# Performance work log

Measured on AMD Instinct MI355X. Metric: run time of the kernel, lower is better.

The kernel has to match this reference:

```python
import jax, jax.numpy as jnp
import numpy as np

BLOCK_SIZES = [256] * 8            # sum = N_CTX = 2048
B, H, D = 2, 16, 64
N_CTX = sum(BLOCK_SIZES)
SPARSITY_PATTERN = 'block_causal'  # row_starts = 0, row_ends = end of own block


def _build_masks(block_sizes, pattern):
    cs = np.cumsum([0] + list(block_sizes))
    row_ends = np.concatenate([np.full(bs, cs[i + 1], dtype=np.int32)
                               for i, bs in enumerate(block_sizes)])
    if pattern == 'block_diagonal':
        row_starts = np.concatenate([np.full(bs, cs[i], dtype=np.int32)
                                     for i, bs in enumerate(block_sizes)])
    elif pattern == 'block_causal':
        row_starts = np.zeros_like(row_ends)
    else:
        raise ValueError(pattern)
    return jnp.asarray(row_starts), jnp.asarray(row_ends)


def setup_inputs() -> dict:
    key = jax.random.key(0)
    kq, kk, kv = jax.random.split(key, 3)
    q = jax.random.normal(kq, (B, H, N_CTX, D), dtype=jnp.float32)
    k = jax.random.normal(kk, (B, H, N_CTX, D), dtype=jnp.float32)
    v = jax.random.normal(kv, (B, H, N_CTX, D), dtype=jnp.float32)
    row_starts, row_ends = _build_masks(BLOCK_SIZES, SPARSITY_PATTERN)
    sm_scale = jnp.float32(1.0 / np.sqrt(D))
    return {"q": q, "k": k, "v": v, "sm_scale": sm_scale,
            "row_starts": row_starts, "row_ends": row_ends}


def reference(q, k, v, sm_scale, row_starts, row_ends):
    # q,k,v: [B,H,N,D]; per query row i, attend to kv cols in [row_starts[i], row_ends[i])
    n = q.shape[2]
    cols = jnp.arange(n, dtype=jnp.int32)
    allowed = (cols[None, :] >= row_starts[:, None]) & (cols[None, :] < row_ends[:, None])  # [N,N]
    scores = jnp.einsum('bhqd,bhkd->bhqk', q, k) * sm_scale
    neg = jnp.finfo(scores.dtype).min
    scores = jnp.where(allowed[None, None], scores, neg)
    p = jax.nn.softmax(scores, axis=-1)
    return jnp.einsum('bhqk,bhkd->bhqd', p, v)
```

## Files before the change

kernel.cpp:

```cpp
#include <hip/hip_runtime.h>


typedef short bf16x8 __attribute__((ext_vector_type(8)));
typedef float f32x4  __attribute__((ext_vector_type(4)));
typedef unsigned short u16;
typedef u16 u16x8 __attribute__((ext_vector_type(8)));

#define MFMA(A,B,C) __builtin_amdgcn_mfma_f32_16x16x32_bf16((A),(B),(C),0,0,0)

__device__ __forceinline__ u16 f2bf_rne(float f) {
    union { float f; unsigned u; } c; c.f = f;
    unsigned r = c.u + 0x7FFFu + ((c.u >> 16) & 1u);
    return (u16)(r >> 16);
}
__device__ __forceinline__ u16 f2bf_fast(float f) {
    union { float f; unsigned u; } c; c.f = f;
    return (u16)((c.u + 0x8000u) >> 16);
}

__global__ __launch_bounds__(256, 2)
void bsattn_fused(const float* __restrict__ Q, const float* __restrict__ K,
                  const float* __restrict__ V, const float* __restrict__ SC,
                  const int* __restrict__ RS, const int* __restrict__ RE,
                  float* __restrict__ O)
{
    constexpr int N = 2048, D = 64;
    int wg = blockIdx.x;
    int bh = wg & 31;
    int i0 = wg >> 5;
    int qsub = (i0 < 8) ? i0 : 23 - i0;
    int q0 = qsub << 7;

    int tid = threadIdx.x, wid = tid >> 6, lane = tid & 63;
    int n = lane & 15, g = lane >> 4;

    __shared__ __align__(16) u16 lsm[16384];
    __shared__ int sbi[8];

    int row0 = q0 + wid * 32 + n;
    int row1 = row0 + 16;
    int rs_l0 = RS[row0], re_l0 = RE[row0];
    int rs_l1 = RS[row1], re_l1 = RE[row1];
    int w_rs_min = min(rs_l0, rs_l1), w_rs_max = max(rs_l0, rs_l1);
    int w_re_min = min(re_l0, re_l1), w_re_max = max(re_l0, re_l1);
    #pragma unroll
    for (int o = 1; o < 16; o <<= 1) {
        w_rs_min = min(w_rs_min, __shfl_xor(w_rs_min, o));
        w_rs_max = max(w_rs_max, __shfl_xor(w_rs_max, o));
        w_re_min = min(w_re_min, __shfl_xor(w_re_min, o));
        w_re_max = max(w_re_max, __shfl_xor(w_re_max, o));
    }
    if (lane == 0) { sbi[wid * 2] = w_rs_min; sbi[wid * 2 + 1] = w_re_max; }

    float sscale = SC[0] * 1.44269504088896340736f;

    bf16x8 qA0, qA1, qB0, qB1;
    {
        const float* qp = Q + ((size_t)bh * N + row0) * D + g * 8;
        float4 a0 = *(const float4*)qp,        a1 = *(const float4*)(qp + 4);
        float4 b0 = *(const float4*)(qp + 32), b1 = *(const float4*)(qp + 36);
        qA0[0]=f2bf_rne(a0.x*sscale); qA0[1]=f2bf_rne(a0.y*sscale);
        qA0[2]=f2bf_rne(a0.z*sscale); qA0[3]=f2bf_rne(a0.w*sscale);
        qA0[4]=f2bf_rne(a1.x*sscale); qA0[5]=f2bf_rne(a1.y*sscale);
        qA0[6]=f2bf_rne(a1.z*sscale); qA0[7]=f2bf_rne(a1.w*sscale);
        qA1[0]=f2bf_rne(b0.x*sscale); qA1[1]=f2bf_rne(b0.y*sscale);
        qA1[2]=f2bf_rne(b0.z*sscale); qA1[3]=f2bf_rne(b0.w*sscale);
        qA1[4]=f2bf_rne(b1.x*sscale); qA1[5]=f2bf_rne(b1.y*sscale);
        qA1[6]=f2bf_rne(b1.z*sscale); qA1[7]=f2bf_rne(b1.w*sscale);
    }
    {
        const float* qp = Q + ((size_t)bh * N + row1) * D + g * 8;
        float4 a0 = *(const float4*)qp,        a1 = *(const float4*)(qp + 4);
        float4 b0 = *(const float4*)(qp + 32), b1 = *(const float4*)(qp + 36);
        qB0[0]=f2bf_rne(a0.x*sscale); qB0[1]=f2bf_rne(a0.y*sscale);
        qB0[2]=f2bf_rne(a0.z*sscale); qB0[3]=f2bf_rne(a0.w*sscale);
        qB0[4]=f2bf_rne(a1.x*sscale); qB0[5]=f2bf_rne(a1.y*sscale);
        qB0[6]=f2bf_rne(a1.z*sscale); qB0[7]=f2bf_rne(a1.w*sscale);
        qB1[0]=f2bf_rne(b0.x*sscale); qB1[1]=f2bf_rne(b0.y*sscale);
        qB1[2]=f2bf_rne(b0.z*sscale); qB1[3]=f2bf_rne(b0.w*sscale);
        qB1[4]=f2bf_rne(b1.x*sscale); qB1[5]=f2bf_rne(b1.y*sscale);
        qB1[6]=f2bf_rne(b1.z*sscale); qB1[7]=f2bf_rne(b1.w*sscale);
    }

    __syncthreads();
    int kst  = min(min(sbi[0], sbi[2]), min(sbi[4], sbi[6])) & ~63;
    int kend = max(max(sbi[1], sbi[3]), max(sbi[5], sbi[7]));
    int t0 = kst >> 6;
    int w  = (kend - kst + 63) >> 6;

    int rA   = ((n >> 2) << 3) + (n & 3);
    int phk  = (n & 3) + 4 * ((n >> 2) & 1);
    int osA0 = rA * 64 + ((g + phk) & 7) * 8;
    int osA1 = rA * 64 + ((g + 4 + phk) & 7) * 8;
    int ov0  = 4096 + n * 64 + ((    g + (n & 7)) & 7) * 8;
    int ov1  = 4096 + n * 64 + ((4 + g + (n & 7)) & 7) * 8;

    int key_l = tid >> 2, c2 = (tid & 3) << 1;
    int rotb  = (key_l & 3) + 4 * ((key_l >> 3) & 1);
    int kiA   = key_l * 64 + (((c2    ) + rotb) & 7) * 8;
    int kiB   = key_l * 64 + (((c2 + 1) + rotb) & 7) * 8;
    int kc    = lane >> 3, kw = lane & 7;
    const float* Kb = K + (size_t)bh * N * D;
    const float* Vb = V + (size_t)bh * N * D;

    f32x4 accA[4], accB[4];
    f32x4 acclA = {0.f,0.f,0.f,0.f}, acclB = {0.f,0.f,0.f,0.f};
    #pragma unroll
    for (int c = 0; c < 4; ++c) {
        accA[c] = (f32x4){0.f,0.f,0.f,0.f};
        accB[c] = (f32x4){0.f,0.f,0.f,0.f};
    }
    bf16x8 ones;
    #pragma unroll
    for (int j = 0; j < 8; ++j) ones[j] = (short)0x3F80;

    float4 kf0, kf1, kf2, kf3, vf0, vf1, vf2, vf3;

    auto stage_load = [&](int i) {
        if (i < w) {
            const float* kp = Kb + (size_t)(t0 + i) * 4096 + key_l * 64 + c2 * 8;
            kf0 = *(const float4*)kp;       kf1 = *(const float4*)(kp + 4);
            kf2 = *(const float4*)(kp + 8); kf3 = *(const float4*)(kp + 12);
            const float* vp = Vb + (size_t)(t0 + i) * 4096 + lane * 64 + wid * 16;
            vf0 = *(const float4*)vp;       vf1 = *(const float4*)(vp + 4);
            vf2 = *(const float4*)(vp + 8); vf3 = *(const float4*)(vp + 12);
        }
    };
    auto stage_write = [&](int i) {
        if (i < w) {
            u16* dst = &lsm[(i & 1) << 13];
            u16x8 a, b;
            a[0]=f2bf_rne(kf0.x); a[1]=f2bf_rne(kf0.y); a[2]=f2bf_rne(kf0.z); a[3]=f2bf_rne(kf0.w);
            a[4]=f2bf_rne(kf1.x); a[5]=f2bf_rne(kf1.y); a[6]=f2bf_rne(kf1.z); a[7]=f2bf_rne(kf1.w);
            b[0]=f2bf_rne(kf2.x); b[1]=f2bf_rne(kf2.y); b[2]=f2bf_rne(kf2.z); b[3]=f2bf_rne(kf2.w);
            b[4]=f2bf_rne(kf3.x); b[5]=f2bf_rne(kf3.y); b[6]=f2bf_rne(kf3.z); b[7]=f2bf_rne(kf3.w);
            *(u16x8*)&dst[kiA] = a;
            *(u16x8*)&dst[kiB] = b;
            float vy[16] = { vf0.x,vf0.y,vf0.z,vf0.w, vf1.x,vf1.y,vf1.z,vf1.w,
                             vf2.x,vf2.y,vf2.z,vf2.w, vf3.x,vf3.y,vf3.z,vf3.w };
            #pragma unroll
            for (int j = 0; j < 16; ++j) {
                int d = wid * 16 + j;
                dst[4096 + d * 64 + ((kc + (j & 7)) & 7) * 8 + kw] = f2bf_rne(vy[j]);
            }
        }
    };

    auto proc = [&](int kb, const u16* ls) {
        bool bdry = (kb < w_rs_max) || (kb + 64 > w_re_min);
        #pragma unroll
        for (int h = 0; h < 2; ++h) {
            int hb = h * 2048;
            bf16x8 k00 = *(const bf16x8*)&ls[hb + osA0];
            bf16x8 k01 = *(const bf16x8*)&ls[hb + osA1];
            bf16x8 k10 = *(const bf16x8*)&ls[hb + osA0 + 256];
            bf16x8 k11 = *(const bf16x8*)&ls[hb + osA1 + 256];
            f32x4 tA0 = {0.f,0.f,0.f,0.f}, tA1 = tA0, tB0 = tA0, tB1 = tA0;
            __builtin_amdgcn_s_setprio(1);
            tA0 = MFMA(k00, qA0, tA0); tA0 = MFMA(k01, qA1, tA0);
            tA1 = MFMA(k10, qA0, tA1); tA1 = MFMA(k11, qA1, tA1);
            tB0 = MFMA(k00, qB0, tB0); tB0 = MFMA(k01, qB1, tB0);
            tB1 = MFMA(k10, qB0, tB1); tB1 = MFMA(k11, qB1, tB1);
            __builtin_amdgcn_s_setprio(0);
            float sA[8], sB[8];
            #pragma unroll
            for (int r = 0; r < 4; ++r) {
                sA[r] = tA0[r]; sA[4 + r] = tA1[r];
                sB[r] = tB0[r]; sB[4 + r] = tB1[r];
            }
            if (bdry) {
                #pragma unroll
                for (int j = 0; j < 8; ++j) {
                    int key = kb + h * 32 + g * 8 + j;
                    if (key < rs_l0 || key >= re_l0) sA[j] = -1e30f;
                    if (key < rs_l1 || key >= re_l1) sB[j] = -1e30f;
                }
            }
            bf16x8 pA, pB;
            #pragma unroll
            for (int j = 0; j < 8; ++j) { float p = __builtin_amdgcn_exp2f(sA[j]); pA[j] = (short)f2bf_fast(p); }
            #pragma unroll
            for (int j = 0; j < 8; ++j) { float p = __builtin_amdgcn_exp2f(sB[j]); pB[j] = (short)f2bf_fast(p); }
            int ov = h ? ov1 : ov0;
            bf16x8 v0 = *(const bf16x8*)&ls[ov       ];
            bf16x8 v1 = *(const bf16x8*)&ls[ov + 1024];
            bf16x8 v2 = *(const bf16x8*)&ls[ov + 2048];
            bf16x8 v3 = *(const bf16x8*)&ls[ov + 3072];
            __builtin_amdgcn_s_setprio(1);
            accA[0] = MFMA(pA, v0, accA[0]);
            accA[1] = MFMA(pA, v1, accA[1]);
            accA[2] = MFMA(pA, v2, accA[2]);
            accA[3] = MFMA(pA, v3, accA[3]);
            acclA   = MFMA(pA, ones, acclA);
            accB[0] = MFMA(pB, v0, accB[0]);
            accB[1] = MFMA(pB, v1, accB[1]);
            accB[2] = MFMA(pB, v2, accB[2]);
            accB[3] = MFMA(pB, v3, accB[3]);
            acclB   = MFMA(pB, ones, acclB);
            __builtin_amdgcn_s_setprio(0);
        }
    };

    stage_load(0);
    stage_write(0);
    stage_load(1);
    for (int i = 0; i < w; ++i) {
        __syncthreads();
        proc(kst + (i << 6), &lsm[(i & 1) << 13]);
        stage_write(i + 1);
        stage_load(i + 2);
    }

    int rb = g << 2;
    {
        int orow = q0 + wid * 32 + rb;
        float* ob = O + ((size_t)bh * N + orow) * D + n;
        #pragma unroll
        for (int r = 0; r < 4; ++r) {
            float li = 1.0f / acclA[r];
            float* rp = ob + (size_t)r * D;
            rp[0]  = accA[0][r] * li;
            rp[16] = accA[1][r] * li;
            rp[32] = accA[2][r] * li;
            rp[48] = accA[3][r] * li;
        }
    }
    {
        int orow = q0 + wid * 32 + 16 + rb;
        float* ob = O + ((size_t)bh * N + orow) * D + n;
        #pragma unroll
        for (int r = 0; r < 4; ++r) {
            float li = 1.0f / acclB[r];
            float* rp = ob + (size_t)r * D;
            rp[0]  = accB[0][r] * li;
            rp[16] = accB[1][r] * li;
            rp[32] = accB[2][r] * li;
            rp[48] = accB[3][r] * li;
        }
    }
}

extern "C" void kernel_launch(void* const* d_in, const int* in_sizes, int n_in,
                              void* d_out, int out_size, void* d_ws, size_t ws_size,
                              hipStream_t stream) {
    const float* q  = (const float*)d_in[0];
    const float* k  = (const float*)d_in[1];
    const float* v  = (const float*)d_in[2];
    const float* sc = (const float*)d_in[3];
    const int* rs   = (const int*)d_in[4];
    const int* re   = (const int*)d_in[5];
    float* out      = (float*)d_out;

    bsattn_fused<<<dim3(512), dim3(256), 0, stream>>>(q, k, v, sc, rs, re, out);
}
```

Before: 130.8 us.

## Halve query tile to 64 rows, double grid, raise occupancy, reorder tile schedule

Each workgroup now handles 64 query rows (16 per wave) instead of 128, so the grid grows from 512 to 1024 workgroups and launch bounds ask for 4 blocks per CU. The tile order is remapped to put the longest causal query tiles first, which is meant to balance load. The prefetch depth in the K/V pipeline drops from two stages ahead to one, and each wave now holds a single Q fragment and one set of accumulators, which lowers register pressure. The cost is that every K/V tile is loaded and converted by twice as many workgroups, roughly doubling global traffic and conversion work per output row, and the shorter prefetch distance gives less time to hide load latency.

```diff
diff --git a/kernel.cpp b/kernel.cpp
--- a/kernel.cpp
+++ b/kernel.cpp
@@ -18,7 +18,7 @@
     return (u16)((c.u + 0x8000u) >> 16);
 }
 
-__global__ __launch_bounds__(256, 2)
+__global__ __launch_bounds__(256, 4)
 void bsattn_fused(const float* __restrict__ Q, const float* __restrict__ K,
                   const float* __restrict__ V, const float* __restrict__ SC,
                   const int* __restrict__ RS, const int* __restrict__ RE,
@@ -27,9 +27,11 @@
     constexpr int N = 2048, D = 64;
     int wg = blockIdx.x;
     int bh = wg & 31;
-    int i0 = wg >> 5;
-    int qsub = (i0 < 8) ? i0 : 23 - i0;
-    int q0 = qsub << 7;
+    int i0 = wg >> 5, kk = i0 & 7, rr = i0 >> 3;
+    int qt = (rr == 0) ? ((kk < 4) ? 28 + kk : 20 + kk)
+           : (rr == 1) ? ((kk < 4) ? 20 + kk : 12 + kk)
+           : (rr == 2) ? (8 + kk) : kk;
+    int q0 = qt << 6;
 
     int tid = threadIdx.x, wid = tid >> 6, lane = tid & 63;
     int n = lane & 15, g = lane >> 4;
@@ -37,12 +39,9 @@
     __shared__ __align__(16) u16 lsm[16384];
     __shared__ int sbi[8];
 
-    int row0 = q0 + wid * 32 + n;
-    int row1 = row0 + 16;
-    int rs_l0 = RS[row0], re_l0 = RE[row0];
-    int rs_l1 = RS[row1], re_l1 = RE[row1];
-    int w_rs_min = min(rs_l0, rs_l1), w_rs_max = max(rs_l0, rs_l1);
-    int w_re_min = min(re_l0, re_l1), w_re_max = max(re_l0, re_l1);
+    int myrow = q0 + wid * 16 + n;
+    int rs_l = RS[myrow], re_l = RE[myrow];
+    int w_rs_min = rs_l, w_rs_max = rs_l, w_re_min = re_l, w_re_max = re_l;
     #pragma unroll
     for (int o = 1; o < 16; o <<= 1) {
         w_rs_min = min(w_rs_min, __shfl_xor(w_rs_min, o));
@@ -54,32 +53,19 @@
 
     float sscale = SC[0] * 1.44269504088896340736f;
 
-    bf16x8 qA0, qA1, qB0, qB1;
+    bf16x8 qf0, qf1;
     {
-        const float* qp = Q + ((size_t)bh * N + row0) * D + g * 8;
+        const float* qp = Q + ((size_t)bh * N + myrow) * D + g * 8;
         float4 a0 = *(const float4*)qp,        a1 = *(const float4*)(qp + 4);
         float4 b0 = *(const float4*)(qp + 32), b1 = *(const float4*)(qp + 36);
-        qA0[0]=f2bf_rne(a0.x*sscale); qA0[1]=f2bf_rne(a0.y*sscale);
-        qA0[2]=f2bf_rne(a0.z*sscale); qA0[3]=f2bf_rne(a0.w*sscale);
-        qA0[4]=f2bf_rne(a1.x*sscale); qA0[5]=f2bf_rne(a1.y*sscale);
-        qA0[6]=f2bf_rne(a1.z*sscale); qA0[7]=f2bf_rne(a1.w*sscale);
-        qA1[0]=f2bf_rne(b0.x*sscale); qA1[1]=f2bf_rne(b0.y*sscale);
-        qA1[2]=f2bf_rne(b0.z*sscale); qA1[3]=f2bf_rne(b0.w*sscale);
-        qA1[4]=f2bf_rne(b1.x*sscale); qA1[5]=f2bf_rne(b1.y*sscale);
-        qA1[6]=f2bf_rne(b1.z*sscale); qA1[7]=f2bf_rne(b1.w*sscale);
-    }
-    {
-        const float* qp = Q + ((size_t)bh * N + row1) * D + g * 8;
-        float4 a0 = *(const float4*)qp,        a1 = *(const float4*)(qp + 4);
-        float4 b0 = *(const float4*)(qp + 32), b1 = *(const float4*)(qp + 36);
-        qB0[0]=f2bf_rne(a0.x*sscale); qB0[1]=f2bf_rne(a0.y*sscale);
-        qB0[2]=f2bf_rne(a0.z*sscale); qB0[3]=f2bf_rne(a0.w*sscale);
-        qB0[4]=f2bf_rne(a1.x*sscale); qB0[5]=f2bf_rne(a1.y*sscale);
-        qB0[6]=f2bf_rne(a1.z*sscale); qB0[7]=f2bf_rne(a1.w*sscale);
-        qB1[0]=f2bf_rne(b0.x*sscale); qB1[1]=f2bf_rne(b0.y*sscale);
-        qB1[2]=f2bf_rne(b0.z*sscale); qB1[3]=f2bf_rne(b0.w*sscale);
-        qB1[4]=f2bf_rne(b1.x*sscale); qB1[5]=f2bf_rne(b1.y*sscale);
-        qB1[6]=f2bf_rne(b1.z*sscale); qB1[7]=f2bf_rne(b1.w*sscale);
+        qf0[0]=f2bf_rne(a0.x*sscale); qf0[1]=f2bf_rne(a0.y*sscale);
+        qf0[2]=f2bf_rne(a0.z*sscale); qf0[3]=f2bf_rne(a0.w*sscale);
+        qf0[4]=f2bf_rne(a1.x*sscale); qf0[5]=f2bf_rne(a1.y*sscale);
+        qf0[6]=f2bf_rne(a1.z*sscale); qf0[7]=f2bf_rne(a1.w*sscale);
+        qf1[0]=f2bf_rne(b0.x*sscale); qf1[1]=f2bf_rne(b0.y*sscale);
+        qf1[2]=f2bf_rne(b0.z*sscale); qf1[3]=f2bf_rne(b0.w*sscale);
+        qf1[4]=f2bf_rne(b1.x*sscale); qf1[5]=f2bf_rne(b1.y*sscale);
+        qf1[6]=f2bf_rne(b1.z*sscale); qf1[7]=f2bf_rne(b1.w*sscale);
     }
 
     __syncthreads();
@@ -103,13 +89,9 @@
     const float* Kb = K + (size_t)bh * N * D;
     const float* Vb = V + (size_t)bh * N * D;
 
-    f32x4 accA[4], accB[4];
-    f32x4 acclA = {0.f,0.f,0.f,0.f}, acclB = {0.f,0.f,0.f,0.f};
-    #pragma unroll
-    for (int c = 0; c < 4; ++c) {
-        accA[c] = (f32x4){0.f,0.f,0.f,0.f};
-        accB[c] = (f32x4){0.f,0.f,0.f,0.f};
-    }
+    f32x4 acc[4], accl = {0.f, 0.f, 0.f, 0.f};
+    #pragma unroll
+    for (int c = 0; c < 4; ++c) acc[c] = (f32x4){0.f, 0.f, 0.f, 0.f};
     bf16x8 ones;
     #pragma unroll
     for (int j = 0; j < 8; ++j) ones[j] = (short)0x3F80;
@@ -147,96 +129,68 @@
     };
 
     auto proc = [&](int kb, const u16* ls) {
-        bool bdry = (kb < w_rs_max) || (kb + 64 > w_re_min);
+        float sc[16];
         #pragma unroll
         for (int h = 0; h < 2; ++h) {
             int hb = h * 2048;
-            bf16x8 k00 = *(const bf16x8*)&ls[hb + osA0];
-            bf16x8 k01 = *(const bf16x8*)&ls[hb + osA1];
-            bf16x8 k10 = *(const bf16x8*)&ls[hb + osA0 + 256];
-            bf16x8 k11 = *(const bf16x8*)&ls[hb + osA1 + 256];
-            f32x4 tA0 = {0.f,0.f,0.f,0.f}, tA1 = tA0, tB0 = tA0, tB1 = tA0;
+            f32x4 t0v = {0.f,0.f,0.f,0.f}, t1v = t0v;
             __builtin_amdgcn_s_setprio(1);
-            tA0 = MFMA(k00, qA0, tA0); tA0 = MFMA(k01, qA1, tA0);
-            tA1 = MFMA(k10, qA0, tA1); tA1 = MFMA(k11, qA1, tA1);
-            tB0 = MFMA(k00, qB0, tB0); tB0 = MFMA(k01, qB1, tB0);
-            tB1 = MFMA(k10, qB0, tB1); tB1 = MFMA(k11, qB1, tB1);
+            t0v = MFMA(*(const bf16x8*)&ls[hb + osA0],       qf0, t0v);
+            t0v = MFMA(*(const bf16x8*)&ls[hb + osA1],       qf1, t0v);
+            t1v = MFMA(*(const bf16x8*)&ls[hb + osA0 + 256], qf0, t1v);
+            t1v = MFMA(*(const bf16x8*)&ls[hb + osA1 + 256], qf1, t1v);
             __builtin_amdgcn_s_setprio(0);
-            float sA[8], sB[8];
             #pragma unroll
-            for (int r = 0; r < 4; ++r) {
-                sA[r] = tA0[r]; sA[4 + r] = tA1[r];
-                sB[r] = tB0[r]; sB[4 + r] = tB1[r];
-            }
-            if (bdry) {
+            for (int r = 0; r < 4; ++r) { sc[h*8 + r] = t0v[r]; sc[h*8 + 4 + r] = t1v[r]; }
+        }
+        if (kb < w_rs_max || kb + 64 > w_re_min) {
+            #pragma unroll
+            for (int h = 0; h < 2; ++h)
                 #pragma unroll
                 for (int j = 0; j < 8; ++j) {
                     int key = kb + h * 32 + g * 8 + j;
-                    if (key < rs_l0 || key >= re_l0) sA[j] = -1e30f;
-                    if (key < rs_l1 || key >= re_l1) sB[j] = -1e30f;
+                    if (key < rs_l || key >= re_l) sc[h*8 + j] = -1e30f;
                 }
-            }
-            bf16x8 pA, pB;
-            #pragma unroll
-            for (int j = 0; j < 8; ++j) { float p = __builtin_amdgcn_exp2f(sA[j]); pA[j] = (short)f2bf_fast(p); }
-            #pragma unroll
-            for (int j = 0; j < 8; ++j) { float p = __builtin_amdgcn_exp2f(sB[j]); pB[j] = (short)f2bf_fast(p); }
+        }
+        bf16x8 pf0, pf1;
+        #pragma unroll
+        for (int j = 0; j < 8; ++j) { float p = __builtin_amdgcn_exp2f(sc[j]);     pf0[j] = (short)f2bf_fast(p); }
+        #pragma unroll
+        for (int j = 0; j < 8; ++j) { float p = __builtin_amdgcn_exp2f(sc[8 + j]); pf1[j] = (short)f2bf_fast(p); }
+        #pragma unroll
+        for (int h = 0; h < 2; ++h) {
+            const bf16x8& pf = h ? pf1 : pf0;
             int ov = h ? ov1 : ov0;
-            bf16x8 v0 = *(const bf16x8*)&ls[ov       ];
-            bf16x8 v1 = *(const bf16x8*)&ls[ov + 1024];
-            bf16x8 v2 = *(const bf16x8*)&ls[ov + 2048];
-            bf16x8 v3 = *(const bf16x8*)&ls[ov + 3072];
             __builtin_amdgcn_s_setprio(1);
-            accA[0] = MFMA(pA, v0, accA[0]);
-            accA[1] = MFMA(pA, v1, accA[1]);
-            accA[2] = MFMA(pA, v2, accA[2]);
-            accA[3] = MFMA(pA, v3, accA[3]);
-            acclA   = MFMA(pA, ones, acclA);
-            accB[0] = MFMA(pB, v0, accB[0]);
-            accB[1] = MFMA(pB, v1, accB[1]);
-            accB[2] = MFMA(pB, v2, accB[2]);
-            accB[3] = MFMA(pB, v3, accB[3]);
-            acclB   = MFMA(pB, ones, acclB);
+            acc[0] = MFMA(pf, *(const bf16x8*)&ls[ov       ], acc[0]);
+            acc[1] = MFMA(pf, *(const bf16x8*)&ls[ov + 1024], acc[1]);
+            acc[2] = MFMA(pf, *(const bf16x8*)&ls[ov + 2048], acc[2]);
+            acc[3] = MFMA(pf, *(const bf16x8*)&ls[ov + 3072], acc[3]);
+            accl   = MFMA(pf, ones, accl);
             __builtin_amdgcn_s_setprio(0);
         }
     };
 
     stage_load(0);
     stage_write(0);
-    stage_load(1);
     for (int i = 0; i < w; ++i) {
         __syncthreads();
+        stage_load(i + 1);
         proc(kst + (i << 6), &lsm[(i & 1) << 13]);
         stage_write(i + 1);
-        stage_load(i + 2);
     }
 
     int rb = g << 2;
-    {
-        int orow = q0 + wid * 32 + rb;
-        float* ob = O + ((size_t)bh * N + orow) * D + n;
-        #pragma unroll
-        for (int r = 0; r < 4; ++r) {
-            float li = 1.0f / acclA[r];
-            float* rp = ob + (size_t)r * D;
-            rp[0]  = accA[0][r] * li;
-            rp[16] = accA[1][r] * li;
-            rp[32] = accA[2][r] * li;
-            rp[48] = accA[3][r] * li;
-        }
-    }
-    {
-        int orow = q0 + wid * 32 + 16 + rb;
-        float* ob = O + ((size_t)bh * N + orow) * D + n;
-        #pragma unroll
-        for (int r = 0; r < 4; ++r) {
-            float li = 1.0f / acclB[r];
-            float* rp = ob + (size_t)r * D;
-            rp[0]  = accB[0][r] * li;
-            rp[16] = accB[1][r] * li;
-            rp[32] = accB[2][r] * li;
-            rp[48] = accB[3][r] * li;
-        }
+    int orow = q0 + wid * 16 + rb;
+    float* ob = O + ((size_t)bh * N + orow) * D + n;
+    #pragma unroll
+    for (int r = 0; r < 4; ++r) {
+        float li = 1.0f / accl[r];
+        float* rp = ob + (size_t)r * D;
+        rp[0]  = acc[0][r] * li;
+        rp[16] = acc[1][r] * li;
+        rp[32] = acc[2][r] * li;
+        rp[48] = acc[3][r] * li;
     }
 }
 
@@ -251,5 +205,5 @@
     const int* re   = (const int*)d_in[5];
     float* out      = (float*)d_out;
 
-    bsattn_fused<<<dim3(512), dim3(256), 0, stream>>>(q, k, v, sc, rs, re, out);
-}
+    bsattn_fused<<<dim3(1024), dim3(256), 0, stream>>>(q, k, v, sc, rs, re, out);
+}
```

After: 141.1 us. 1.08x slower.
